# Performance work log

Measured on AMD Instinct MI355X. Metric: run time of the kernel, lower is better.

## Reference

```python
import jax, jax.numpy as jnp
import numpy as np
import math

NUM_LEVEL = 16
LEVEL_DIM = 2
BASE_RES = 16
LOG2_T = 19
LEVEL_SCALE = 1.38191288
N_POINTS = 262144

_PRIMES = np.array([1, 2654435761, 805459861], dtype=np.uint32)  # tiny-cuda-nn hash primes
_CORNERS = np.array([[(c >> d) & 1 for d in range(3)] for c in range(8)], dtype=np.uint32)  # [8,3]


def _grid_meta():
    # mirrors GridEncoder.get_grid_info: per-level table offsets (aligned to 8)
    max_len = 2 ** LOG2_T
    offs = []
    off = 0
    for i in range(NUM_LEVEL):
        res = int(np.ceil(BASE_RES * LEVEL_SCALE ** i))
        p = min(max_len, res ** 3)
        p = int(np.ceil(p / 8) * 8)
        offs.append(off)
        off += p
    offs.append(off)
    return offs


def setup_inputs() -> dict:
    key = jax.random.key(0)
    k1, k2 = jax.random.split(key)
    offs = _grid_meta()
    # raw coords in [-1, 1); forward maps (x+1)/2 -> [0, 1)
    input_means = jax.random.uniform(k1, (N_POINTS, 3), dtype=jnp.float32) * 2.0 - 1.0
    # embeddings.data.uniform_(-0.01, 0.01)
    embeddings = jax.random.uniform(k2, (offs[-1], LEVEL_DIM), dtype=jnp.float32) * 0.02 - 0.01
    return {"input_means": input_means, "embeddings": embeddings}


def _encode(input_means, embeddings):
    x = (input_means + 1.0) / 2.0  # [N,3] in [0,1]
    offs = _grid_meta()
    lg_scale = math.log2(LEVEL_SCALE)
    corners = jnp.asarray(_CORNERS)  # [8,3]
    primes = jnp.asarray(_PRIMES)    # [3]
    outs = []
    for l in range(NUM_LEVEL):
        hsize = offs[l + 1] - offs[l]                    # table rows this level
        scale = 2.0 ** (l * lg_scale) * BASE_RES - 1.0   # align_corners=True
        res = int(math.ceil(scale)) + 1                  # grid resolution
        table = embeddings[offs[l]:offs[l + 1]]          # [hsize, C]
        pos = x * scale                                  # align_corners -> no +0.5
        pg = jnp.floor(pos)
        frac = pos - pg                                  # [N,3]
        pgu = pg.astype(jnp.uint32)
        cpos = pgu[:, None, :] + corners[None]           # [N,8,3] corner coords
        if res ** 3 > hsize:
            # hashed level: xor of coord*prime (uint32 wraparound)
            h = cpos * primes
            idx = h[..., 0] ^ h[..., 1] ^ h[..., 2]
        else:
            # dense (tiled) level
            r = jnp.uint32(res)
            idx = cpos[..., 0] + cpos[..., 1] * r + cpos[..., 2] * r * r
        idx = (idx % jnp.uint32(hsize)).astype(jnp.int32)
        feats = table[idx]                               # [N,8,C] gather
        w = jnp.where(corners[None] == 1, frac[:, None, :], 1.0 - frac[:, None, :]).prod(-1)  # [N,8]
        outs.append(jnp.einsum('nk,nkc->nc', w, feats))  # trilinear interp
    # matches ot_encod.permute(1,0,2).reshape(N, L*C): level-major feature concat
    return jnp.concatenate(outs, axis=-1)                # [N, L*C]


def reference(input_means, embeddings):
    return _encode(input_means, embeddings)
```

## Files before the change

kernel.cpp:

```cpp
#include <hip/hip_runtime.h>
#include <cmath>

#define NPTS 262144
#define NLVL 16
#define NDENSE 5
#define NHASH 11
#define HASH_MASK 0x7FFFFu
#define P2 2654435761u
#define P3 805459861u

typedef float v2f __attribute__((ext_vector_type(2)));
typedef float v4f __attribute__((ext_vector_type(4)));

struct MetaD { float scale[NDENSE]; unsigned off[NDENSE]; unsigned res[NDENSE]; };
struct MetaH { float scale[NHASH]; unsigned off[NHASH]; };

struct Pt { float x, y, z; };
struct Prep { unsigned idx[8]; float fx, fy, fz; };

__device__ __forceinline__ Pt load_pt(const float* __restrict__ means, int p) {
    Pt q;
    q.x = (__builtin_nontemporal_load(means + 3 * p + 0) + 1.0f) * 0.5f;
    q.y = (__builtin_nontemporal_load(means + 3 * p + 1) + 1.0f) * 0.5f;
    q.z = (__builtin_nontemporal_load(means + 3 * p + 2) + 1.0f) * 0.5f;
    return q;
}

__device__ __forceinline__ Prep dprep(Pt q, float s, unsigned r, unsigned off) {
    const float px = q.x * s, py = q.y * s, pz = q.z * s;
    const float gx = floorf(px), gy = floorf(py), gz = floorf(pz);
    Prep d;
    d.fx = px - gx; d.fy = py - gy; d.fz = pz - gz;
    const unsigned dy = r, dz = r * r;
    const unsigned base = (unsigned)gx + (unsigned)gy * dy + (unsigned)gz * dz + off;
    d.idx[0] = base;           d.idx[1] = base + 1;
    d.idx[2] = base + dy;      d.idx[3] = base + dy + 1;
    d.idx[4] = base + dz;      d.idx[5] = base + dz + 1;
    d.idx[6] = base + dz + dy; d.idx[7] = base + dz + dy + 1;
    return d;
}

__device__ __forceinline__ Prep hprep(Pt q, float s, unsigned off) {
    const float px = q.x * s, py = q.y * s, pz = q.z * s;
    const float gx = floorf(px), gy = floorf(py), gz = floorf(pz);
    Prep d;
    d.fx = px - gx; d.fy = py - gy; d.fz = pz - gz;
    const unsigned ix = (unsigned)gx, iy = (unsigned)gy, iz = (unsigned)gz;
    const unsigned hy0 = iy * P2, hy1 = hy0 + P2;
    const unsigned hz0 = iz * P3, hz1 = hz0 + P3;
    const unsigned h0 = hy0 ^ hz0, h1 = hy1 ^ hz0, h2 = hy0 ^ hz1, h3 = hy1 ^ hz1;
    d.idx[0] = ((ix ^ h0) & HASH_MASK) + off; d.idx[1] = (((ix + 1u) ^ h0) & HASH_MASK) + off;
    d.idx[2] = ((ix ^ h1) & HASH_MASK) + off; d.idx[3] = (((ix + 1u) ^ h1) & HASH_MASK) + off;
    d.idx[4] = ((ix ^ h2) & HASH_MASK) + off; d.idx[5] = (((ix + 1u) ^ h2) & HASH_MASK) + off;
    d.idx[6] = ((ix ^ h3) & HASH_MASK) + off; d.idx[7] = (((ix + 1u) ^ h3) & HASH_MASK) + off;
    return d;
}

__device__ __forceinline__ v2f trilerp(const v2f* f, float fx, float fy, float fz) {
    const float wx0 = 1.0f - fx, wy0 = 1.0f - fy, wz0 = 1.0f - fz;
    const float w00 = wz0 * wy0, w01 = wz0 * fy, w10 = fz * wy0, w11 = fz * fy;
    return w00 * (wx0 * f[0] + fx * f[1]) + w01 * (wx0 * f[2] + fx * f[3])
         + w10 * (wx0 * f[4] + fx * f[5]) + w11 * (wx0 * f[6] + fx * f[7]);
}

__global__ __launch_bounds__(256) void enc_dense(
    const float* __restrict__ means, const float* __restrict__ emb,
    v2f* __restrict__ dst, int lvl_major, MetaD meta)
{
    const int l = blockIdx.y;
    const int p0 = blockIdx.x * 512 + threadIdx.x;
    const float s = meta.scale[l];
    const unsigned off = meta.off[l];
    const unsigned r = meta.res[l];
    const v2f* __restrict__ emb2 = (const v2f*)emb;

    const Prep A = dprep(load_pt(means, p0), s, r, off);
    v2f fa[8];
#pragma unroll
    for (int k = 0; k < 8; ++k) fa[k] = emb2[A.idx[k]];
    const Prep B = dprep(load_pt(means, p0 + 256), s, r, off);
    v2f fb[8];
#pragma unroll
    for (int k = 0; k < 8; ++k) fb[k] = emb2[B.idx[k]];

    const v2f ra = trilerp(fa, A.fx, A.fy, A.fz);
    const size_t diA = lvl_major ? ((size_t)l * NPTS + p0) : ((size_t)p0 * NLVL + l);
    __builtin_nontemporal_store(ra, &dst[diA]);
    const v2f rb = trilerp(fb, B.fx, B.fy, B.fz);
    const size_t diB = lvl_major ? ((size_t)l * NPTS + p0 + 256) : ((size_t)(p0 + 256) * NLVL + l);
    __builtin_nontemporal_store(rb, &dst[diB]);
}

__global__ __launch_bounds__(256) void enc_hash(
    const float* __restrict__ means, const float* __restrict__ emb,
    v2f* __restrict__ dst, int lvl_major, MetaH meta)
{
    const unsigned b = blockIdx.x;
    const unsigned xcd = b & 7u, slot = b >> 3;
    unsigned il, chunk;
    if (slot < 512u) { il = xcd; chunk = slot; }
    else {
        const unsigned g = xcd * 192u + (slot - 512u);
        il = 8u + (g >> 9);
        chunk = g & 511u;
    }
    const float s = meta.scale[il];
    const unsigned off = meta.off[il];
    const unsigned lvl = il + NDENSE;
    const int p0 = (int)(chunk * 512u + threadIdx.x);
    const v2f* __restrict__ emb2 = (const v2f*)emb;

    const Prep A = hprep(load_pt(means, p0), s, off);
    v2f fa[8];
#pragma unroll
    for (int k = 0; k < 8; ++k) fa[k] = emb2[A.idx[k]];
    const Prep B = hprep(load_pt(means, p0 + 256), s, off);
    v2f fb[8];
#pragma unroll
    for (int k = 0; k < 8; ++k) fb[k] = emb2[B.idx[k]];

    const v2f ra = trilerp(fa, A.fx, A.fy, A.fz);
    const size_t diA = lvl_major ? ((size_t)lvl * NPTS + p0) : ((size_t)p0 * NLVL + lvl);
    __builtin_nontemporal_store(ra, &dst[diA]);
    const v2f rb = trilerp(fb, B.fx, B.fy, B.fz);
    const size_t diB = lvl_major ? ((size_t)lvl * NPTS + (p0 + 256)) : ((size_t)(p0 + 256) * NLVL + lvl);
    __builtin_nontemporal_store(rb, &dst[diB]);
}

__global__ __launch_bounds__(256) void transpose_out(
    const v2f* __restrict__ ws, float* __restrict__ out)
{
    const int p = blockIdx.x * 256 + threadIdx.x;
    v4f o[8];
    v2f* o2 = (v2f*)o;
#pragma unroll
    for (int l = 0; l < NLVL; ++l)
        o2[l] = __builtin_nontemporal_load(&ws[(size_t)l * NPTS + p]);
    v4f* out4 = (v4f*)(out + (size_t)p * (2 * NLVL));
#pragma unroll
    for (int k = 0; k < 8; ++k)
        __builtin_nontemporal_store(o[k], &out4[k]);
}

extern "C" void kernel_launch(void* const* d_in, const int* in_sizes, int n_in,
                              void* d_out, int out_size, void* d_ws, size_t ws_size,
                              hipStream_t stream)
{
    const float* means = (const float*)d_in[0];
    const float* emb   = (const float*)d_in[1];
    float* out         = (float*)d_out;

    MetaD md;
    MetaH mh;
    const double lg = log2(1.38191288);
    unsigned off = 0;
    for (int l = 0; l < NLVL; ++l) {
        const double scale_d = pow(2.0, (double)l * lg) * 16.0 - 1.0;
        const unsigned res_enc = (unsigned)ceil(scale_d) + 1u;

        const double gres_d = ceil(16.0 * pow(1.38191288, (double)l));
        unsigned long long r3 = (unsigned long long)gres_d;
        r3 = r3 * r3 * r3;
        unsigned long long pl = r3 < (1ull << 19) ? r3 : (1ull << 19);
        pl = (pl + 7ull) / 8ull * 8ull;

        if (l < NDENSE) {
            md.scale[l] = (float)scale_d;
            md.off[l]   = off;
            md.res[l]   = res_enc;
        } else {
            mh.scale[l - NDENSE] = (float)scale_d;
            mh.off[l - NDENSE]   = off;
        }
        off += (unsigned)pl;
    }

    const size_t ws_needed = (size_t)NLVL * NPTS * sizeof(float) * 2;
    const bool use_ws = ws_size >= ws_needed;
    v2f* dst = use_ws ? (v2f*)d_ws : (v2f*)out;
    const int lvl_major = use_ws ? 1 : 0;

    enc_dense<<<dim3(NPTS / 512, NDENSE, 1), 256, 0, stream>>>(means, emb, dst, lvl_major, md);
    enc_hash <<<dim3(8 * 704, 1, 1),          256, 0, stream>>>(means, emb, dst, lvl_major, mh);
    if (use_ws)
        transpose_out<<<NPTS / 256, 256, 0, stream>>>((const v2f*)d_ws, out);
}
```

Measured before the change: 247.2 us.

## Pair x-adjacent corner gathers into 16-byte loads for dense and hashed levels

Dense levels now fetch each x-adjacent corner pair with one 16-byte (8-byte aligned) load, halving gather instructions. Hashed levels rely on the fact that x and x+1 share a 16-byte aligned pair when x is even, since XOR with the yz hash leaves the pair together. They issue one aligned v4 load per yz corner plus four extra loads only when x is odd, then pick lanes by parity. Nontemporal loads and stores are replaced with normal ones, and the weight products are precomputed. The added cost is divergence on odd-x lanes and extra lane-select logic.

```diff
diff --git a/kernel.cpp b/kernel.cpp
--- a/kernel.cpp
+++ b/kernel.cpp
@@ -11,56 +11,68 @@
 
 typedef float v2f __attribute__((ext_vector_type(2)));
 typedef float v4f __attribute__((ext_vector_type(4)));
+typedef float v4f8 __attribute__((ext_vector_type(4), aligned(8)));
 
 struct MetaD { float scale[NDENSE]; unsigned off[NDENSE]; unsigned res[NDENSE]; };
 struct MetaH { float scale[NHASH]; unsigned off[NHASH]; };
 
 struct Pt { float x, y, z; };
-struct Prep { unsigned idx[8]; float fx, fy, fz; };
 
 __device__ __forceinline__ Pt load_pt(const float* __restrict__ means, int p) {
     Pt q;
-    q.x = (__builtin_nontemporal_load(means + 3 * p + 0) + 1.0f) * 0.5f;
-    q.y = (__builtin_nontemporal_load(means + 3 * p + 1) + 1.0f) * 0.5f;
-    q.z = (__builtin_nontemporal_load(means + 3 * p + 2) + 1.0f) * 0.5f;
+    q.x = (means[3 * p + 0] + 1.0f) * 0.5f;
+    q.y = (means[3 * p + 1] + 1.0f) * 0.5f;
+    q.z = (means[3 * p + 2] + 1.0f) * 0.5f;
     return q;
 }
 
-__device__ __forceinline__ Prep dprep(Pt q, float s, unsigned r, unsigned off) {
+struct PrepD { unsigned b[4]; float fx; float wc[4]; };
+
+__device__ __forceinline__ PrepD dprep(Pt q, float s, unsigned r, unsigned off) {
     const float px = q.x * s, py = q.y * s, pz = q.z * s;
     const float gx = floorf(px), gy = floorf(py), gz = floorf(pz);
-    Prep d;
-    d.fx = px - gx; d.fy = py - gy; d.fz = pz - gz;
+    const float fx = px - gx, fy = py - gy, fz = pz - gz;
     const unsigned dy = r, dz = r * r;
     const unsigned base = (unsigned)gx + (unsigned)gy * dy + (unsigned)gz * dz + off;
-    d.idx[0] = base;           d.idx[1] = base + 1;
-    d.idx[2] = base + dy;      d.idx[3] = base + dy + 1;
-    d.idx[4] = base + dz;      d.idx[5] = base + dz + 1;
-    d.idx[6] = base + dz + dy; d.idx[7] = base + dz + dy + 1;
+    PrepD d;
+    d.b[0] = base; d.b[1] = base + dy; d.b[2] = base + dz; d.b[3] = base + dz + dy;
+    d.fx = fx;
+    const float wy0 = 1.0f - fy, wz0 = 1.0f - fz;
+    d.wc[0] = wz0 * wy0; d.wc[1] = wz0 * fy; d.wc[2] = fz * wy0; d.wc[3] = fz * fy;
     return d;
 }
 
-__device__ __forceinline__ Prep hprep(Pt q, float s, unsigned off) {
+struct PrepH { unsigned hyz[4]; unsigned e, odd; float fx; float wc[4]; };
+
+__device__ __forceinline__ PrepH hprep(Pt q, float s) {
     const float px = q.x * s, py = q.y * s, pz = q.z * s;
     const float gx = floorf(px), gy = floorf(py), gz = floorf(pz);
-    Prep d;
-    d.fx = px - gx; d.fy = py - gy; d.fz = pz - gz;
+    const float fx = px - gx, fy = py - gy, fz = pz - gz;
     const unsigned ix = (unsigned)gx, iy = (unsigned)gy, iz = (unsigned)gz;
+    PrepH d;
     const unsigned hy0 = iy * P2, hy1 = hy0 + P2;
     const unsigned hz0 = iz * P3, hz1 = hz0 + P3;
-    const unsigned h0 = hy0 ^ hz0, h1 = hy1 ^ hz0, h2 = hy0 ^ hz1, h3 = hy1 ^ hz1;
-    d.idx[0] = ((ix ^ h0) & HASH_MASK) + off; d.idx[1] = (((ix + 1u) ^ h0) & HASH_MASK) + off;
-    d.idx[2] = ((ix ^ h1) & HASH_MASK) + off; d.idx[3] = (((ix + 1u) ^ h1) & HASH_MASK) + off;
-    d.idx[4] = ((ix ^ h2) & HASH_MASK) + off; d.idx[5] = (((ix + 1u) ^ h2) & HASH_MASK) + off;
-    d.idx[6] = ((ix ^ h3) & HASH_MASK) + off; d.idx[7] = (((ix + 1u) ^ h3) & HASH_MASK) + off;
+    d.hyz[0] = hy0 ^ hz0; d.hyz[1] = hy1 ^ hz0; d.hyz[2] = hy0 ^ hz1; d.hyz[3] = hy1 ^ hz1;
+    d.e = ix & ~1u; d.odd = ix & 1u;
+    d.fx = fx;
+    const float wy0 = 1.0f - fy, wz0 = 1.0f - fz;
+    d.wc[0] = wz0 * wy0; d.wc[1] = wz0 * fy; d.wc[2] = fz * wy0; d.wc[3] = fz * fy;
     return d;
 }
 
-__device__ __forceinline__ v2f trilerp(const v2f* f, float fx, float fy, float fz) {
-    const float wx0 = 1.0f - fx, wy0 = 1.0f - fy, wz0 = 1.0f - fz;
-    const float w00 = wz0 * wy0, w01 = wz0 * fy, w10 = fz * wy0, w11 = fz * fy;
-    return w00 * (wx0 * f[0] + fx * f[1]) + w01 * (wx0 * f[2] + fx * f[3])
-         + w10 * (wx0 * f[4] + fx * f[5]) + w11 * (wx0 * f[6] + fx * f[7]);
+__device__ __forceinline__ v2f hfinish(const PrepH& d, const v4f* F, const v2f* G) {
+    const float wx0 = 1.0f - d.fx;
+    v2f acc = {0.0f, 0.0f};
+#pragma unroll
+    for (int c = 0; c < 4; ++c) {
+        const v2f lo = {F[c].x, F[c].y};
+        const v2f hi = {F[c].z, F[c].w};
+        const bool sw = ((d.hyz[c] ^ d.odd) & 1u) != 0u;
+        const v2f c0 = sw ? hi : lo;
+        const v2f c1 = d.odd ? G[c] : (sw ? lo : hi);
+        acc += d.wc[c] * (wx0 * c0 + d.fx * c1);
+    }
+    return acc;
 }
 
 __global__ __launch_bounds__(256) void enc_dense(
@@ -72,23 +84,26 @@
     const float s = meta.scale[l];
     const unsigned off = meta.off[l];
     const unsigned r = meta.res[l];
-    const v2f* __restrict__ emb2 = (const v2f*)emb;
-
-    const Prep A = dprep(load_pt(means, p0), s, r, off);
-    v2f fa[8];
-#pragma unroll
-    for (int k = 0; k < 8; ++k) fa[k] = emb2[A.idx[k]];
-    const Prep B = dprep(load_pt(means, p0 + 256), s, r, off);
-    v2f fb[8];
-#pragma unroll
-    for (int k = 0; k < 8; ++k) fb[k] = emb2[B.idx[k]];
-
-    const v2f ra = trilerp(fa, A.fx, A.fy, A.fz);
+
+    const PrepD A = dprep(load_pt(means, p0), s, r, off);
+    const PrepD B = dprep(load_pt(means, p0 + 256), s, r, off);
+    v4f8 FA[4], FB[4];
+#pragma unroll
+    for (int c = 0; c < 4; ++c) FA[c] = *(const v4f8*)(emb + 2u * A.b[c]);
+#pragma unroll
+    for (int c = 0; c < 4; ++c) FB[c] = *(const v4f8*)(emb + 2u * B.b[c]);
+
+    v2f ra = {0.0f, 0.0f}, rb = {0.0f, 0.0f};
+    const float ax0 = 1.0f - A.fx, bx0 = 1.0f - B.fx;
+#pragma unroll
+    for (int c = 0; c < 4; ++c) {
+        ra += A.wc[c] * (ax0 * (v2f){FA[c].x, FA[c].y} + A.fx * (v2f){FA[c].z, FA[c].w});
+        rb += B.wc[c] * (bx0 * (v2f){FB[c].x, FB[c].y} + B.fx * (v2f){FB[c].z, FB[c].w});
+    }
     const size_t diA = lvl_major ? ((size_t)l * NPTS + p0) : ((size_t)p0 * NLVL + l);
-    __builtin_nontemporal_store(ra, &dst[diA]);
-    const v2f rb = trilerp(fb, B.fx, B.fy, B.fz);
+    dst[diA] = ra;
     const size_t diB = lvl_major ? ((size_t)l * NPTS + p0 + 256) : ((size_t)(p0 + 256) * NLVL + l);
-    __builtin_nontemporal_store(rb, &dst[diB]);
+    dst[diB] = rb;
 }
 
 __global__ __launch_bounds__(256) void enc_hash(
@@ -110,21 +125,38 @@
     const int p0 = (int)(chunk * 512u + threadIdx.x);
     const v2f* __restrict__ emb2 = (const v2f*)emb;
 
-    const Prep A = hprep(load_pt(means, p0), s, off);
-    v2f fa[8];
-#pragma unroll
-    for (int k = 0; k < 8; ++k) fa[k] = emb2[A.idx[k]];
-    const Prep B = hprep(load_pt(means, p0 + 256), s, off);
-    v2f fb[8];
-#pragma unroll
-    for (int k = 0; k < 8; ++k) fb[k] = emb2[B.idx[k]];
-
-    const v2f ra = trilerp(fa, A.fx, A.fy, A.fz);
+    const PrepH A = hprep(load_pt(means, p0), s);
+    const PrepH B = hprep(load_pt(means, p0 + 256), s);
+
+    v4f FA[4], FB[4];
+#pragma unroll
+    for (int c = 0; c < 4; ++c) {
+        const unsigned a = (A.e ^ A.hyz[c]) & HASH_MASK;
+        FA[c] = *(const v4f*)(emb + 2u * (off + (a & ~1u)));
+    }
+#pragma unroll
+    for (int c = 0; c < 4; ++c) {
+        const unsigned a = (B.e ^ B.hyz[c]) & HASH_MASK;
+        FB[c] = *(const v4f*)(emb + 2u * (off + (a & ~1u)));
+    }
+    v2f GA[4] = {}, GB[4] = {};
+    if (A.odd) {
+#pragma unroll
+        for (int c = 0; c < 4; ++c)
+            GA[c] = emb2[off + (((A.e + 2u) ^ A.hyz[c]) & HASH_MASK)];
+    }
+    if (B.odd) {
+#pragma unroll
+        for (int c = 0; c < 4; ++c)
+            GB[c] = emb2[off + (((B.e + 2u) ^ B.hyz[c]) & HASH_MASK)];
+    }
+
+    const v2f ra = hfinish(A, FA, GA);
     const size_t diA = lvl_major ? ((size_t)lvl * NPTS + p0) : ((size_t)p0 * NLVL + lvl);
-    __builtin_nontemporal_store(ra, &dst[diA]);
-    const v2f rb = trilerp(fb, B.fx, B.fy, B.fz);
+    dst[diA] = ra;
+    const v2f rb = hfinish(B, FB, GB);
     const size_t diB = lvl_major ? ((size_t)lvl * NPTS + (p0 + 256)) : ((size_t)(p0 + 256) * NLVL + lvl);
-    __builtin_nontemporal_store(rb, &dst[diB]);
+    dst[diB] = rb;
 }
 
 __global__ __launch_bounds__(256) void transpose_out(
```

Result: no change. 251.1 us (+1.6%).

## Fuse dense-level encoding into the transpose/finalize kernel

Applied to the files above, without the earlier changes.

The separate dense-level kernel goes away and the five dense levels are now computed inside the final transpose kernel, which also reads the hash-level results from the workspace. The workspace no longer carries the dense levels' round trip or one kernel launch. Hash-kernel stores to the workspace change from nontemporal to normal so the finalize pass may hit them in cache. The cost is more gather work and register pressure in the finalize kernel, which runs with fewer threads in flight per level.

```diff
diff --git a/kernel.cpp b/kernel.cpp
--- a/kernel.cpp
+++ b/kernel.cpp
@@ -18,26 +18,12 @@
 struct Pt { float x, y, z; };
 struct Prep { unsigned idx[8]; float fx, fy, fz; };
 
-__device__ __forceinline__ Pt load_pt(const float* __restrict__ means, int p) {
+__device__ __forceinline__ Pt load_pt_nt(const float* __restrict__ means, int p) {
     Pt q;
     q.x = (__builtin_nontemporal_load(means + 3 * p + 0) + 1.0f) * 0.5f;
     q.y = (__builtin_nontemporal_load(means + 3 * p + 1) + 1.0f) * 0.5f;
     q.z = (__builtin_nontemporal_load(means + 3 * p + 2) + 1.0f) * 0.5f;
     return q;
-}
-
-__device__ __forceinline__ Prep dprep(Pt q, float s, unsigned r, unsigned off) {
-    const float px = q.x * s, py = q.y * s, pz = q.z * s;
-    const float gx = floorf(px), gy = floorf(py), gz = floorf(pz);
-    Prep d;
-    d.fx = px - gx; d.fy = py - gy; d.fz = pz - gz;
-    const unsigned dy = r, dz = r * r;
-    const unsigned base = (unsigned)gx + (unsigned)gy * dy + (unsigned)gz * dz + off;
-    d.idx[0] = base;           d.idx[1] = base + 1;
-    d.idx[2] = base + dy;      d.idx[3] = base + dy + 1;
-    d.idx[4] = base + dz;      d.idx[5] = base + dz + 1;
-    d.idx[6] = base + dz + dy; d.idx[7] = base + dz + dy + 1;
-    return d;
 }
 
 __device__ __forceinline__ Prep hprep(Pt q, float s, unsigned off) {
@@ -63,34 +49,6 @@
          + w10 * (wx0 * f[4] + fx * f[5]) + w11 * (wx0 * f[6] + fx * f[7]);
 }
 
-__global__ __launch_bounds__(256) void enc_dense(
-    const float* __restrict__ means, const float* __restrict__ emb,
-    v2f* __restrict__ dst, int lvl_major, MetaD meta)
-{
-    const int l = blockIdx.y;
-    const int p0 = blockIdx.x * 512 + threadIdx.x;
-    const float s = meta.scale[l];
-    const unsigned off = meta.off[l];
-    const unsigned r = meta.res[l];
-    const v2f* __restrict__ emb2 = (const v2f*)emb;
-
-    const Prep A = dprep(load_pt(means, p0), s, r, off);
-    v2f fa[8];
-#pragma unroll
-    for (int k = 0; k < 8; ++k) fa[k] = emb2[A.idx[k]];
-    const Prep B = dprep(load_pt(means, p0 + 256), s, r, off);
-    v2f fb[8];
-#pragma unroll
-    for (int k = 0; k < 8; ++k) fb[k] = emb2[B.idx[k]];
-
-    const v2f ra = trilerp(fa, A.fx, A.fy, A.fz);
-    const size_t diA = lvl_major ? ((size_t)l * NPTS + p0) : ((size_t)p0 * NLVL + l);
-    __builtin_nontemporal_store(ra, &dst[diA]);
-    const v2f rb = trilerp(fb, B.fx, B.fy, B.fz);
-    const size_t diB = lvl_major ? ((size_t)l * NPTS + p0 + 256) : ((size_t)(p0 + 256) * NLVL + l);
-    __builtin_nontemporal_store(rb, &dst[diB]);
-}
-
 __global__ __launch_bounds__(256) void enc_hash(
     const float* __restrict__ means, const float* __restrict__ emb,
     v2f* __restrict__ dst, int lvl_major, MetaH meta)
@@ -110,32 +68,93 @@
     const int p0 = (int)(chunk * 512u + threadIdx.x);
     const v2f* __restrict__ emb2 = (const v2f*)emb;
 
-    const Prep A = hprep(load_pt(means, p0), s, off);
+    const Prep A = hprep(load_pt_nt(means, p0), s, off);
     v2f fa[8];
 #pragma unroll
     for (int k = 0; k < 8; ++k) fa[k] = emb2[A.idx[k]];
-    const Prep B = hprep(load_pt(means, p0 + 256), s, off);
+    const Prep B = hprep(load_pt_nt(means, p0 + 256), s, off);
     v2f fb[8];
 #pragma unroll
     for (int k = 0; k < 8; ++k) fb[k] = emb2[B.idx[k]];
 
     const v2f ra = trilerp(fa, A.fx, A.fy, A.fz);
     const size_t diA = lvl_major ? ((size_t)lvl * NPTS + p0) : ((size_t)p0 * NLVL + lvl);
-    __builtin_nontemporal_store(ra, &dst[diA]);
+    dst[diA] = ra;
     const v2f rb = trilerp(fb, B.fx, B.fy, B.fz);
     const size_t diB = lvl_major ? ((size_t)lvl * NPTS + (p0 + 256)) : ((size_t)(p0 + 256) * NLVL + lvl);
-    __builtin_nontemporal_store(rb, &dst[diB]);
-}
-
-__global__ __launch_bounds__(256) void transpose_out(
-    const v2f* __restrict__ ws, float* __restrict__ out)
+    dst[diB] = rb;
+}
+
+__global__ __launch_bounds__(256) void enc_dense(
+    const float* __restrict__ means, const float* __restrict__ emb,
+    v2f* __restrict__ dst, int lvl_major, MetaD meta)
 {
     const int p = blockIdx.x * 256 + threadIdx.x;
+    const int l = blockIdx.y;
+
+    const float x = (means[3 * p + 0] + 1.0f) * 0.5f;
+    const float y = (means[3 * p + 1] + 1.0f) * 0.5f;
+    const float z = (means[3 * p + 2] + 1.0f) * 0.5f;
+
+    const float s = meta.scale[l];
+    const unsigned off = meta.off[l];
+    const unsigned r = meta.res[l];
+
+    const float px = x * s, py = y * s, pz = z * s;
+    const float gx = floorf(px), gy = floorf(py), gz = floorf(pz);
+    const float fx = px - gx, fy = py - gy, fz = pz - gz;
+    const unsigned base = (unsigned)gx + (unsigned)gy * r + (unsigned)gz * r * r + off;
+    const unsigned dy = r, dz = r * r;
+
+    const v2f* __restrict__ emb2 = (const v2f*)emb;
+    v2f f[8];
+    f[0] = emb2[base];           f[1] = emb2[base + 1];
+    f[2] = emb2[base + dy];      f[3] = emb2[base + dy + 1];
+    f[4] = emb2[base + dz];      f[5] = emb2[base + dz + 1];
+    f[6] = emb2[base + dz + dy]; f[7] = emb2[base + dz + dy + 1];
+
+    const v2f res = trilerp(f, fx, fy, fz);
+    const size_t di = lvl_major ? ((size_t)l * NPTS + p) : ((size_t)p * NLVL + l);
+    dst[di] = res;
+}
+
+__global__ __launch_bounds__(256) void finalize(
+    const float* __restrict__ means, const float* __restrict__ emb,
+    const v2f* __restrict__ ws, float* __restrict__ out, MetaD meta)
+{
+    const int p = blockIdx.x * 256 + threadIdx.x;
+
+    v2f h[NHASH];
+#pragma unroll
+    for (int l = 0; l < NHASH; ++l)
+        h[l] = __builtin_nontemporal_load(&ws[(size_t)(NDENSE + l) * NPTS + p]);
+
+    const Pt q = load_pt_nt(means, p);
+
     v4f o[8];
     v2f* o2 = (v2f*)o;
 #pragma unroll
-    for (int l = 0; l < NLVL; ++l)
-        o2[l] = __builtin_nontemporal_load(&ws[(size_t)l * NPTS + p]);
+    for (int l = 0; l < NDENSE; ++l) {
+        const float s = meta.scale[l];
+        const unsigned off = meta.off[l];
+        const unsigned r = meta.res[l];
+        const float px = q.x * s, py = q.y * s, pz = q.z * s;
+        const float gx = floorf(px), gy = floorf(py), gz = floorf(pz);
+        const float fx = px - gx, fy = py - gy, fz = pz - gz;
+        const unsigned base = (unsigned)gx + (unsigned)gy * r + (unsigned)gz * r * r + off;
+        const unsigned dy = r, dz = r * r;
+        const v2f* __restrict__ emb2 = (const v2f*)emb;
+        v2f f[8];
+        f[0] = emb2[base];           f[1] = emb2[base + 1];
+        f[2] = emb2[base + dy];      f[3] = emb2[base + dy + 1];
+        f[4] = emb2[base + dz];      f[5] = emb2[base + dz + 1];
+        f[6] = emb2[base + dz + dy]; f[7] = emb2[base + dz + dy + 1];
+        o2[l] = trilerp(f, fx, fy, fz);
+    }
+#pragma unroll
+    for (int l = 0; l < NHASH; ++l)
+        o2[NDENSE + l] = h[l];
+
     v4f* out4 = (v4f*)(out + (size_t)p * (2 * NLVL));
 #pragma unroll
     for (int k = 0; k < 8; ++k)
@@ -177,11 +196,14 @@
 
     const size_t ws_needed = (size_t)NLVL * NPTS * sizeof(float) * 2;
     const bool use_ws = ws_size >= ws_needed;
-    v2f* dst = use_ws ? (v2f*)d_ws : (v2f*)out;
-    const int lvl_major = use_ws ? 1 : 0;
-
-    enc_dense<<<dim3(NPTS / 512, NDENSE, 1), 256, 0, stream>>>(means, emb, dst, lvl_major, md);
-    enc_hash <<<dim3(8 * 704, 1, 1),          256, 0, stream>>>(means, emb, dst, lvl_major, mh);
-    if (use_ws)
-        transpose_out<<<NPTS / 256, 256, 0, stream>>>((const v2f*)d_ws, out);
-}
+
+    if (use_ws) {
+        v2f* wsp = (v2f*)d_ws;
+        enc_hash<<<dim3(8 * 704, 1, 1), 256, 0, stream>>>(means, emb, wsp, 1, mh);
+        finalize<<<NPTS / 256, 256, 0, stream>>>(means, emb, (const v2f*)wsp, out, md);
+    } else {
+        v2f* dst = (v2f*)out;
+        enc_dense<<<dim3(NPTS / 256, NDENSE, 1), 256, 0, stream>>>(means, emb, dst, 0, md);
+        enc_hash <<<dim3(8 * 704, 1, 1),          256, 0, stream>>>(means, emb, dst, 0, mh);
+    }
+}
```

Result: faster. 210.7 us (-14.8%).

## Merge dense and hash encoding kernels into one XCD-aware launch

Applied to the files above, without the earlier changes.

Replaces the separate dense-level and hash-level kernels with a single kernel whose block index is mapped to levels and point chunks, so that hash levels are pinned to particular XCDs and dense levels are spread over the remaining slots. Dense-level blocks handle 1024 points across two passes. This removes one kernel launch and the tail between the two kernels, and is meant to keep each XCD's L2 working on a few hash tables. Encoder output stores change from nontemporal to regular stores. The cost is a more complicated block-to-work mapping, plus some imbalance because dense blocks carry twice the work of hash blocks.

```diff
diff --git a/kernel.cpp b/kernel.cpp
--- a/kernel.cpp
+++ b/kernel.cpp
@@ -4,7 +4,6 @@
 #define NPTS 262144
 #define NLVL 16
 #define NDENSE 5
-#define NHASH 11
 #define HASH_MASK 0x7FFFFu
 #define P2 2654435761u
 #define P3 805459861u
@@ -12,32 +11,17 @@
 typedef float v2f __attribute__((ext_vector_type(2)));
 typedef float v4f __attribute__((ext_vector_type(4)));
 
-struct MetaD { float scale[NDENSE]; unsigned off[NDENSE]; unsigned res[NDENSE]; };
-struct MetaH { float scale[NHASH]; unsigned off[NHASH]; };
+struct MetaU { float scale[NLVL]; unsigned off[NLVL]; unsigned res[NDENSE]; };
 
 struct Pt { float x, y, z; };
 struct Prep { unsigned idx[8]; float fx, fy, fz; };
 
-__device__ __forceinline__ Pt load_pt(const float* __restrict__ means, int p) {
+__device__ __forceinline__ Pt load_pt_nt(const float* __restrict__ means, int p) {
     Pt q;
     q.x = (__builtin_nontemporal_load(means + 3 * p + 0) + 1.0f) * 0.5f;
     q.y = (__builtin_nontemporal_load(means + 3 * p + 1) + 1.0f) * 0.5f;
     q.z = (__builtin_nontemporal_load(means + 3 * p + 2) + 1.0f) * 0.5f;
     return q;
-}
-
-__device__ __forceinline__ Prep dprep(Pt q, float s, unsigned r, unsigned off) {
-    const float px = q.x * s, py = q.y * s, pz = q.z * s;
-    const float gx = floorf(px), gy = floorf(py), gz = floorf(pz);
-    Prep d;
-    d.fx = px - gx; d.fy = py - gy; d.fz = pz - gz;
-    const unsigned dy = r, dz = r * r;
-    const unsigned base = (unsigned)gx + (unsigned)gy * dy + (unsigned)gz * dz + off;
-    d.idx[0] = base;           d.idx[1] = base + 1;
-    d.idx[2] = base + dy;      d.idx[3] = base + dy + 1;
-    d.idx[4] = base + dz;      d.idx[5] = base + dz + 1;
-    d.idx[6] = base + dz + dy; d.idx[7] = base + dz + dy + 1;
-    return d;
 }
 
 __device__ __forceinline__ Prep hprep(Pt q, float s, unsigned off) {
@@ -56,6 +40,20 @@
     return d;
 }
 
+__device__ __forceinline__ Prep dprep(Pt q, float s, unsigned r, unsigned off) {
+    const float px = q.x * s, py = q.y * s, pz = q.z * s;
+    const float gx = floorf(px), gy = floorf(py), gz = floorf(pz);
+    Prep d;
+    d.fx = px - gx; d.fy = py - gy; d.fz = pz - gz;
+    const unsigned dy = r, dz = r * r;
+    const unsigned base = (unsigned)gx + (unsigned)gy * dy + (unsigned)gz * dz + off;
+    d.idx[0] = base;           d.idx[1] = base + 1;
+    d.idx[2] = base + dy;      d.idx[3] = base + dy + 1;
+    d.idx[4] = base + dz;      d.idx[5] = base + dz + 1;
+    d.idx[6] = base + dz + dy; d.idx[7] = base + dz + dy + 1;
+    return d;
+}
+
 __device__ __forceinline__ v2f trilerp(const v2f* f, float fx, float fy, float fz) {
     const float wx0 = 1.0f - fx, wy0 = 1.0f - fy, wz0 = 1.0f - fz;
     const float w00 = wz0 * wy0, w01 = wz0 * fy, w10 = fz * wy0, w11 = fz * fy;
@@ -63,68 +61,68 @@
          + w10 * (wx0 * f[4] + fx * f[5]) + w11 * (wx0 * f[6] + fx * f[7]);
 }
 
-__global__ __launch_bounds__(256) void enc_dense(
+__global__ __launch_bounds__(256) void encode_all(
     const float* __restrict__ means, const float* __restrict__ emb,
-    v2f* __restrict__ dst, int lvl_major, MetaD meta)
-{
-    const int l = blockIdx.y;
-    const int p0 = blockIdx.x * 512 + threadIdx.x;
-    const float s = meta.scale[l];
-    const unsigned off = meta.off[l];
-    const unsigned r = meta.res[l];
-    const v2f* __restrict__ emb2 = (const v2f*)emb;
-
-    const Prep A = dprep(load_pt(means, p0), s, r, off);
-    v2f fa[8];
-#pragma unroll
-    for (int k = 0; k < 8; ++k) fa[k] = emb2[A.idx[k]];
-    const Prep B = dprep(load_pt(means, p0 + 256), s, r, off);
-    v2f fb[8];
-#pragma unroll
-    for (int k = 0; k < 8; ++k) fb[k] = emb2[B.idx[k]];
-
-    const v2f ra = trilerp(fa, A.fx, A.fy, A.fz);
-    const size_t diA = lvl_major ? ((size_t)l * NPTS + p0) : ((size_t)p0 * NLVL + l);
-    __builtin_nontemporal_store(ra, &dst[diA]);
-    const v2f rb = trilerp(fb, B.fx, B.fy, B.fz);
-    const size_t diB = lvl_major ? ((size_t)l * NPTS + p0 + 256) : ((size_t)(p0 + 256) * NLVL + l);
-    __builtin_nontemporal_store(rb, &dst[diB]);
-}
-
-__global__ __launch_bounds__(256) void enc_hash(
-    const float* __restrict__ means, const float* __restrict__ emb,
-    v2f* __restrict__ dst, int lvl_major, MetaH meta)
+    v2f* __restrict__ dst, int lvl_major, MetaU meta)
 {
     const unsigned b = blockIdx.x;
     const unsigned xcd = b & 7u, slot = b >> 3;
-    unsigned il, chunk;
-    if (slot < 512u) { il = xcd; chunk = slot; }
+    unsigned lvl, base_pt;
+    if (slot < 512u) { lvl = 5u + xcd; base_pt = slot * 512u; }
     else {
-        const unsigned g = xcd * 192u + (slot - 512u);
-        il = 8u + (g >> 9);
-        chunk = g & 511u;
+        const unsigned t = slot - 512u;
+        if (xcd < 6u && t < 256u) {
+            lvl = 13u + (xcd >> 1);
+            base_pt = (((xcd & 1u) << 8) + t) * 512u;
+        } else {
+            const unsigned dj = (xcd < 6u) ? (xcd * 96u + (t - 256u))
+                                           : (576u + (xcd - 6u) * 352u + t);
+            lvl = dj >> 8;
+            base_pt = (dj & 255u) * 1024u;
+        }
     }
-    const float s = meta.scale[il];
-    const unsigned off = meta.off[il];
-    const unsigned lvl = il + NDENSE;
-    const int p0 = (int)(chunk * 512u + threadIdx.x);
+    const float s = meta.scale[lvl];
+    const unsigned off = meta.off[lvl];
     const v2f* __restrict__ emb2 = (const v2f*)emb;
 
-    const Prep A = hprep(load_pt(means, p0), s, off);
-    v2f fa[8];
+    if (lvl < NDENSE) {
+        const unsigned r = meta.res[lvl];
+        for (unsigned pass = 0; pass < 2u; ++pass) {
+            const int p0 = (int)(base_pt + pass * 512u + threadIdx.x);
+            const Prep A = dprep(load_pt_nt(means, p0), s, r, off);
+            v2f fa[8];
 #pragma unroll
-    for (int k = 0; k < 8; ++k) fa[k] = emb2[A.idx[k]];
-    const Prep B = hprep(load_pt(means, p0 + 256), s, off);
-    v2f fb[8];
+            for (int k = 0; k < 8; ++k) fa[k] = emb2[A.idx[k]];
+            const Prep B = dprep(load_pt_nt(means, p0 + 256), s, r, off);
+            v2f fb[8];
 #pragma unroll
-    for (int k = 0; k < 8; ++k) fb[k] = emb2[B.idx[k]];
+            for (int k = 0; k < 8; ++k) fb[k] = emb2[B.idx[k]];
 
-    const v2f ra = trilerp(fa, A.fx, A.fy, A.fz);
-    const size_t diA = lvl_major ? ((size_t)lvl * NPTS + p0) : ((size_t)p0 * NLVL + lvl);
-    __builtin_nontemporal_store(ra, &dst[diA]);
-    const v2f rb = trilerp(fb, B.fx, B.fy, B.fz);
-    const size_t diB = lvl_major ? ((size_t)lvl * NPTS + (p0 + 256)) : ((size_t)(p0 + 256) * NLVL + lvl);
-    __builtin_nontemporal_store(rb, &dst[diB]);
+            const v2f ra = trilerp(fa, A.fx, A.fy, A.fz);
+            const size_t diA = lvl_major ? ((size_t)lvl * NPTS + p0) : ((size_t)p0 * NLVL + lvl);
+            dst[diA] = ra;
+            const v2f rb = trilerp(fb, B.fx, B.fy, B.fz);
+            const size_t diB = lvl_major ? ((size_t)lvl * NPTS + (p0 + 256)) : ((size_t)(p0 + 256) * NLVL + lvl);
+            dst[diB] = rb;
+        }
+    } else {
+        const int p0 = (int)(base_pt + threadIdx.x);
+        const Prep A = hprep(load_pt_nt(means, p0), s, off);
+        v2f fa[8];
+#pragma unroll
+        for (int k = 0; k < 8; ++k) fa[k] = emb2[A.idx[k]];
+        const Prep B = hprep(load_pt_nt(means, p0 + 256), s, off);
+        v2f fb[8];
+#pragma unroll
+        for (int k = 0; k < 8; ++k) fb[k] = emb2[B.idx[k]];
+
+        const v2f ra = trilerp(fa, A.fx, A.fy, A.fz);
+        const size_t diA = lvl_major ? ((size_t)lvl * NPTS + p0) : ((size_t)p0 * NLVL + lvl);
+        dst[diA] = ra;
+        const v2f rb = trilerp(fb, B.fx, B.fy, B.fz);
+        const size_t diB = lvl_major ? ((size_t)lvl * NPTS + (p0 + 256)) : ((size_t)(p0 + 256) * NLVL + lvl);
+        dst[diB] = rb;
+    }
 }
 
 __global__ __launch_bounds__(256) void transpose_out(
@@ -150,8 +148,7 @@
     const float* emb   = (const float*)d_in[1];
     float* out         = (float*)d_out;
 
-    MetaD md;
-    MetaH mh;
+    MetaU mu;
     const double lg = log2(1.38191288);
     unsigned off = 0;
     for (int l = 0; l < NLVL; ++l) {
@@ -164,24 +161,20 @@
         unsigned long long pl = r3 < (1ull << 19) ? r3 : (1ull << 19);
         pl = (pl + 7ull) / 8ull * 8ull;
 
-        if (l < NDENSE) {
-            md.scale[l] = (float)scale_d;
-            md.off[l]   = off;
-            md.res[l]   = res_enc;
-        } else {
-            mh.scale[l - NDENSE] = (float)scale_d;
-            mh.off[l - NDENSE]   = off;
-        }
+        mu.scale[l] = (float)scale_d;
+        mu.off[l]   = off;
+        if (l < NDENSE) mu.res[l] = res_enc;
         off += (unsigned)pl;
     }
 
     const size_t ws_needed = (size_t)NLVL * NPTS * sizeof(float) * 2;
     const bool use_ws = ws_size >= ws_needed;
-    v2f* dst = use_ws ? (v2f*)d_ws : (v2f*)out;
-    const int lvl_major = use_ws ? 1 : 0;
 
-    enc_dense<<<dim3(NPTS / 512, NDENSE, 1), 256, 0, stream>>>(means, emb, dst, lvl_major, md);
-    enc_hash <<<dim3(8 * 704, 1, 1),          256, 0, stream>>>(means, emb, dst, lvl_major, mh);
-    if (use_ws)
-        transpose_out<<<NPTS / 256, 256, 0, stream>>>((const v2f*)d_ws, out);
+    if (use_ws) {
+        v2f* wsp = (v2f*)d_ws;
+        encode_all<<<dim3(8 * 864, 1, 1), 256, 0, stream>>>(means, emb, wsp, 1, mu);
+        transpose_out<<<NPTS / 256, 256, 0, stream>>>((const v2f*)wsp, out);
+    } else {
+        encode_all<<<dim3(8 * 864, 1, 1), 256, 0, stream>>>(means, emb, (v2f*)out, 0, mu);
+    }
 }
```

New measurement: 259.1 us. 1.05x slower.
